# Performance work log

Measured on AMD Instinct MI355X. Metric: run time of the kernel, lower is better.

Reference implementation:

```python
import math
import jax, jax.numpy as jnp
import numpy as np

BLOCK_K = 128  # key/value block size; S_k % BLOCK_K == 0 so no padding/mask needed


def setup_inputs() -> dict:
    key = jax.random.key(0)
    kq, kk, kv = jax.random.split(key, 3)
    B, S, H, Hkv, D = 1, 4096, 16, 8, 128
    return {
        "query": jax.random.normal(kq, (B, S, H, D), dtype=jnp.float32),
        "key": jax.random.normal(kk, (B, S, Hkv, D), dtype=jnp.float32),
        "value": jax.random.normal(kv, (B, S, Hkv, D), dtype=jnp.float32),
    }


def _ring_attention(query, key, value, block_k=BLOCK_K):
    # query: [B, Sq, H, D]; key/value: [B, Sk, Hkv, D]
    scale = 1.0 / math.sqrt(query.shape[-1])
    reps = query.shape[2] // key.shape[2]
    if reps > 1:  # GQA: repeat kv heads to match query heads
        key = jnp.repeat(key, reps, axis=2)
        value = jnp.repeat(value, reps, axis=2)
    q = jnp.transpose(query, (0, 2, 1, 3))   # [B, H, Sq, D]
    k = jnp.transpose(key, (0, 2, 1, 3))     # [B, H, Sk, D]
    v = jnp.transpose(value, (0, 2, 1, 3))
    B, H, Sq, D = q.shape
    Sk = k.shape[2]
    nk = Sk // block_k
    # split keys/values into blocks, block axis leading for scan
    kb = k.reshape(B, H, nk, block_k, D).transpose(2, 0, 1, 3, 4)
    vb = v.reshape(B, H, nk, block_k, D).transpose(2, 0, 1, 3, 4)
    m0 = jnp.full((B, H, Sq), -jnp.inf, dtype=jnp.float32)
    l0 = jnp.zeros((B, H, Sq), dtype=jnp.float32)
    o0 = jnp.zeros((B, H, Sq, D), dtype=jnp.float32)

    def step(carry, kv_blk):
        m, l, o = carry
        k_blk, v_blk = kv_blk
        scores = jnp.einsum('bhqd,bhkd->bhqk', q, k_blk) * scale
        m_new = jnp.maximum(m, jnp.max(scores, axis=-1))
        alpha = jnp.exp(m - m_new)                     # rescale factor (0 on first step)
        p = jnp.exp(scores - m_new[..., None])
        l = l * alpha + jnp.sum(p, axis=-1)
        o = o * alpha[..., None] + jnp.einsum('bhqk,bhkd->bhqd', p, v_blk)
        return (m_new, l, o), None

    (m, l, o), _ = jax.lax.scan(step, (m0, l0, o0), (kb, vb))
    out = o / l[..., None]
    return jnp.transpose(out, (0, 2, 1, 3))  # [B, Sq, H, D]


def reference(query, key, value):
    return _ring_attention(query, key, value)
```

## Files before the change

### kernel.cpp

```cpp
#include <hip/hip_runtime.h>
#include <math.h>


namespace {
constexpr int NH  = 16;
constexpr int NKV = 8;
constexpr int DH  = 128;
constexpr int SK  = 4096;
constexpr int TQ  = 128;
constexpr int NTM = 128;
constexpr int NT  = 256;

constexpr int BKM   = 32;
constexpr int NKTM  = SK / BKM;
constexpr int TILEM = BKM * DH;
constexpr size_t WS_NEED = (size_t)2 * NKV * NKTM * TILEM * sizeof(_Float16);

constexpr int NIT   = NKTM / 2;
constexpr int CHUNK = 2 * TILEM;

constexpr int BK  = 64;
constexpr int NKT = SK / BK;

typedef _Float16 half8 __attribute__((ext_vector_type(8)));
typedef _Float16 half4 __attribute__((ext_vector_type(4)));
typedef _Float16 half2v __attribute__((ext_vector_type(2)));
typedef __fp16   fp16x2 __attribute__((ext_vector_type(2)));
typedef float  floatx4 __attribute__((ext_vector_type(4)));
typedef unsigned short ushort8 __attribute__((ext_vector_type(8)));

#define MFMA16(a, b, c) __builtin_amdgcn_mfma_f32_16x16x32_f16((a), (b), (c), 0, 0, 0)

#define BARRIER_LGKM() asm volatile("s_waitcnt lgkmcnt(0)\n\ts_barrier" ::: "memory")

__global__ __launch_bounds__(256)
void prepack_kv(const float* __restrict__ Kg, const float* __restrict__ Vg,
                _Float16* __restrict__ Kx, _Float16* __restrict__ Vx) {
  __shared__ __align__(16) _Float16 Kb[BKM * 128];
  __shared__ __align__(16) _Float16 Vb[BKM * 132];
  const int id = blockIdx.x;
  const int hk = id & 7;
  const int kt = id >> 3;
  const int t  = threadIdx.x;

#pragma unroll
  for (int it = 0; it < 4; ++it) {
    const int r  = it * 8 + (t >> 5);
    const int c4 = t & 31;
    const size_t src = (((size_t)(kt * BKM + r) * NKV + hk) * DH) + c4 * 4;
    const float4 kf = *reinterpret_cast<const float4*>(Kg + src);
    const float4 vf = *reinterpret_cast<const float4*>(Vg + src);
    half4 kh;
    kh[0] = (_Float16)kf.x; kh[1] = (_Float16)kf.y;
    kh[2] = (_Float16)kf.z; kh[3] = (_Float16)kf.w;
    *reinterpret_cast<half4*>(&Kb[r * 128 + c4 * 4]) = kh;
    half2v v0, v1;
    v0[0] = (_Float16)vf.x; v0[1] = (_Float16)vf.y;
    v1[0] = (_Float16)vf.z; v1[1] = (_Float16)vf.w;
    *reinterpret_cast<half2v*>(&Vb[r * 132 + c4 * 4])     = v0;
    *reinterpret_cast<half2v*>(&Vb[r * 132 + c4 * 4 + 2]) = v1;
  }
  __syncthreads();

  {
    _Float16* out = Kx + (size_t)(hk * NKTM + kt) * TILEM;
#pragma unroll
    for (int it = 0; it < 2; ++it) {
      const int L  = it * 2048 + t * 8;
      const int r  = L >> 7;
      const int gp = (L >> 3) & 15;
      const int c8 = gp ^ (r & 7);
      *reinterpret_cast<half8*>(out + L) =
          *reinterpret_cast<const half8*>(&Kb[r * 128 + c8 * 8]);
    }
  }
  {
    _Float16* out = Vx + (size_t)(hk * NKTM + kt) * TILEM;
    const int dp = t >> 2;
    const int g  = t & 3;
    const int ql = g ^ (dp & 3);
    const int d  = dp * 2;
    ushort8 lo, hi;
#pragma unroll
    for (int j = 0; j < 8; ++j) {
      const int key = ((j >> 2) * 16) + ql * 4 + (j & 3);
      const unsigned v = *reinterpret_cast<const unsigned*>(&Vb[key * 132 + d]);
      lo[j] = (unsigned short)(v & 0xffffu);
      hi[j] = (unsigned short)(v >> 16);
    }
    *reinterpret_cast<ushort8*>(out + d * 32 + g * 8)       = lo;
    *reinterpret_cast<ushort8*>(out + (d + 1) * 32 + g * 8) = hi;
  }
}

__global__ __launch_bounds__(NTM, 1)
void flash_fwd_pk(const float* __restrict__ Qg,
                  const _Float16* __restrict__ Kx,
                  const _Float16* __restrict__ Vx,
                  float* __restrict__ Og) {
  __shared__ __align__(16) _Float16 KsB[2][CHUNK];
  __shared__ __align__(16) _Float16 VtB[2][CHUNK];

  const int tid  = threadIdx.x;
  const int wave = tid >> 6;
  const int lane = tid & 63;
  const int m16  = lane & 15;
  const int quad = lane >> 4;
  const int hsw  = m16 & 7;
  const int sw2  = (m16 >> 1) & 3;

  const int id = blockIdx.x;
  const int hk = id & 7;
  const int h  = (hk << 1) | ((id >> 3) & 1);
  const int qt = id >> 4;
  const int qr0 = qt * TQ + wave * 64;

  const float4* Q4 = reinterpret_cast<const float4*>(Qg);
  const float scale2 = (float)(0.08838834764831845 * 1.4426950408889634);

  half8 qa[4][4];
#pragma unroll
  for (int mt = 0; mt < 4; ++mt) {
#pragma unroll
    for (int kc = 0; kc < 4; ++kc) {
      const int r = qr0 + mt * 16 + m16;
      const int b = (r * NH + h) * (DH / 4) + kc * 8 + quad * 2;
      float4 x = Q4[b], y = Q4[b + 1];
      half8 f;
      f[0] = (_Float16)(x.x * scale2); f[1] = (_Float16)(x.y * scale2);
      f[2] = (_Float16)(x.z * scale2); f[3] = (_Float16)(x.w * scale2);
      f[4] = (_Float16)(y.x * scale2); f[5] = (_Float16)(y.y * scale2);
      f[6] = (_Float16)(y.z * scale2); f[7] = (_Float16)(y.w * scale2);
      qa[mt][kc] = f;
    }
  }

  floatx4 o[4][8];
#pragma unroll
  for (int mt = 0; mt < 4; ++mt)
#pragma unroll
    for (int nt = 0; nt < 8; ++nt) o[mt][nt] = (floatx4){0.f, 0.f, 0.f, 0.f};
  float lsum[4] = {0.f, 0.f, 0.f, 0.f};

  const _Float16* gK = Kx + (size_t)hk * NKTM * TILEM;
  const _Float16* gV = Vx + (size_t)hk * NKTM * TILEM;
  const int soff = tid * 8;

  half8 kr[8], vr[8];
#pragma unroll
  for (int i = 0; i < 8; ++i) {
    kr[i] = *reinterpret_cast<const half8*>(gK + i * 1024 + soff);
    vr[i] = *reinterpret_cast<const half8*>(gV + i * 1024 + soff);
  }

  for (int kt = 0; kt < NIT; ++kt) {
    const int b = kt & 1;
#pragma unroll
    for (int i = 0; i < 8; ++i) {
      *reinterpret_cast<half8*>(&KsB[b][i * 1024 + soff]) = kr[i];
      *reinterpret_cast<half8*>(&VtB[b][i * 1024 + soff]) = vr[i];
    }
    {
      const int ktn = (kt + 1 < NIT) ? kt + 1 : kt;
      const _Float16* gKt = gK + (size_t)ktn * CHUNK;
      const _Float16* gVt = gV + (size_t)ktn * CHUNK;
#pragma unroll
      for (int i = 0; i < 8; ++i) {
        kr[i] = *reinterpret_cast<const half8*>(gKt + i * 1024 + soff);
        vr[i] = *reinterpret_cast<const half8*>(gVt + i * 1024 + soff);
      }
    }
    BARRIER_LGKM();

#pragma unroll
    for (int c = 0; c < 2; ++c) {
      const _Float16* Ks = &KsB[b][c * TILEM];
      const _Float16* Vt = &VtB[b][c * TILEM];

      floatx4 s[4][2];
#pragma unroll
      for (int mt = 0; mt < 4; ++mt)
#pragma unroll
        for (int nt = 0; nt < 2; ++nt) s[mt][nt] = (floatx4){0.f, 0.f, 0.f, 0.f};
#pragma unroll
      for (int nt = 0; nt < 2; ++nt) {
#pragma unroll
        for (int kc = 0; kc < 4; ++kc) {
          const int g = (kc * 4 + quad) ^ hsw;
          half8 kb = *reinterpret_cast<const half8*>(
              &Ks[(nt * 16 + m16) * 128 + g * 8]);
          s[0][nt] = MFMA16(kb, qa[0][kc], s[0][nt]);
          s[1][nt] = MFMA16(kb, qa[1][kc], s[1][nt]);
          s[2][nt] = MFMA16(kb, qa[2][kc], s[2][nt]);
          s[3][nt] = MFMA16(kb, qa[3][kc], s[3][nt]);
        }
      }

      union H8 { half8 h; fp16x2 w[4]; };
      half8 pa[4];
#pragma unroll
      for (int mt = 0; mt < 4; ++mt) {
        float p[8];
#pragma unroll
        for (int nt = 0; nt < 2; ++nt)
#pragma unroll
          for (int r = 0; r < 4; ++r)
            p[nt * 4 + r] = __builtin_amdgcn_exp2f(s[mt][nt][r]);
        lsum[mt] += ((p[0] + p[1]) + (p[2] + p[3])) +
                    ((p[4] + p[5]) + (p[6] + p[7]));
        H8 u;
        u.w[0] = __builtin_amdgcn_cvt_pkrtz(p[0], p[1]);
        u.w[1] = __builtin_amdgcn_cvt_pkrtz(p[2], p[3]);
        u.w[2] = __builtin_amdgcn_cvt_pkrtz(p[4], p[5]);
        u.w[3] = __builtin_amdgcn_cvt_pkrtz(p[6], p[7]);
        pa[mt] = u.h;
      }

      const int gq = quad ^ sw2;
#pragma unroll
      for (int nt = 0; nt < 8; ++nt) {
        half8 vb = *reinterpret_cast<const half8*>(
            &Vt[(nt * 16 + m16) * 32 + gq * 8]);
        o[0][nt] = MFMA16(pa[0], vb, o[0][nt]);
        o[1][nt] = MFMA16(pa[1], vb, o[1][nt]);
        o[2][nt] = MFMA16(pa[2], vb, o[2][nt]);
        o[3][nt] = MFMA16(pa[3], vb, o[3][nt]);
      }
    }
  }

#pragma unroll
  for (int mt = 0; mt < 4; ++mt) {
    float ls = lsum[mt];
    ls += __shfl_xor(ls, 16);
    ls += __shfl_xor(ls, 32);
#pragma unroll
    for (int r = 0; r < 4; ++r) {
      const int rq = quad * 4 + r;
      const float inv = 1.f / __shfl(ls, rq);
      const int row = qr0 + mt * 16 + rq;
      const int ob = (row * NH + h) * DH + m16;
#pragma unroll
      for (int nt = 0; nt < 8; ++nt)
        Og[ob + nt * 16] = o[mt][nt][r] * inv;
    }
  }
}

constexpr int KP = 136, VP = 72, PP = 72;

__global__ __launch_bounds__(NT, 2)
void flash_fwd_fb(const float* __restrict__ Qg, const float* __restrict__ Kg,
                  const float* __restrict__ Vg, float* __restrict__ Og) {
  __shared__ _Float16 Ks[BK * KP];
  __shared__ _Float16 Vt[DH * VP];
  __shared__ _Float16 Ps[4 * 32 * PP];

  const int tid  = threadIdx.x;
  const int wave = tid >> 6;
  const int lane = tid & 63;
  const int m16  = lane & 15;
  const int quad = lane >> 4;

  const int id = blockIdx.x;
  const int hk = id & 7;
  const int h  = (hk << 1) | ((id >> 3) & 1);
  const int qt = id >> 4;
  const int qr0 = qt * TQ + wave * 32;

  const float4* Q4 = reinterpret_cast<const float4*>(Qg);
  const float4* K4 = reinterpret_cast<const float4*>(Kg);
  const float scale2 = (float)(0.08838834764831845 * 1.4426950408889634);

  half8 qa[2][4];
#pragma unroll
  for (int mt = 0; mt < 2; ++mt) {
#pragma unroll
    for (int kc = 0; kc < 4; ++kc) {
      const int r = qr0 + mt * 16 + m16;
      const int b = (r * NH + h) * (DH / 4) + kc * 8 + quad * 2;
      float4 x = Q4[b], y = Q4[b + 1];
      half8 f;
      f[0] = (_Float16)(x.x * scale2); f[1] = (_Float16)(x.y * scale2);
      f[2] = (_Float16)(x.z * scale2); f[3] = (_Float16)(x.w * scale2);
      f[4] = (_Float16)(y.x * scale2); f[5] = (_Float16)(y.y * scale2);
      f[6] = (_Float16)(y.z * scale2); f[7] = (_Float16)(y.w * scale2);
      qa[mt][kc] = f;
    }
  }

  floatx4 o[2][8];
#pragma unroll
  for (int mt = 0; mt < 2; ++mt)
#pragma unroll
    for (int nt = 0; nt < 8; ++nt) o[mt][nt] = (floatx4){0.f, 0.f, 0.f, 0.f};
  float lrow[2][4];
#pragma unroll
  for (int mt = 0; mt < 2; ++mt)
#pragma unroll
    for (int r = 0; r < 4; ++r) lrow[mt][r] = 0.f;

  const int kkey = tid >> 2, kdq = tid & 3;
  const int vdim = tid & 127, vkg = tid >> 7;

  float4 kpre[8];
  float  vpre[32];
  {
    const int kb = (kkey * NKV + hk) * (DH / 4);
#pragma unroll
    for (int j = 0; j < 8; ++j) kpre[j] = K4[kb + j * 4 + kdq];
    const int vb = (vkg * 32) * NKV * DH + hk * DH + vdim;
#pragma unroll
    for (int e = 0; e < 32; ++e) vpre[e] = Vg[vb + e * (NKV * DH)];
  }

  for (int kt = 0; kt < NKT; ++kt) {
    __syncthreads();
#pragma unroll
    for (int j = 0; j < 8; ++j) {
      fp16x2 a = __builtin_amdgcn_cvt_pkrtz(kpre[j].x, kpre[j].y);
      fp16x2 b = __builtin_amdgcn_cvt_pkrtz(kpre[j].z, kpre[j].w);
      half4 hv;
      hv[0] = (_Float16)a[0]; hv[1] = (_Float16)a[1];
      hv[2] = (_Float16)b[0]; hv[3] = (_Float16)b[1];
      *reinterpret_cast<half4*>(&Ks[kkey * KP + (j * 4 + kdq) * 4]) = hv;
    }
#pragma unroll
    for (int jj = 0; jj < 4; ++jj) {
      half8 hv;
#pragma unroll
      for (int e = 0; e < 4; ++e) {
        fp16x2 p = __builtin_amdgcn_cvt_pkrtz(vpre[jj * 8 + 2 * e],
                                              vpre[jj * 8 + 2 * e + 1]);
        hv[2 * e] = (_Float16)p[0]; hv[2 * e + 1] = (_Float16)p[1];
      }
      *reinterpret_cast<half8*>(&Vt[vdim * VP + vkg * 32 + jj * 8]) = hv;
    }
    __syncthreads();

    floatx4 s[2][4];
#pragma unroll
    for (int mt = 0; mt < 2; ++mt)
#pragma unroll
      for (int nt = 0; nt < 4; ++nt) s[mt][nt] = (floatx4){0.f, 0.f, 0.f, 0.f};
#pragma unroll
    for (int nt = 0; nt < 4; ++nt) {
#pragma unroll
      for (int kc = 0; kc < 4; ++kc) {
        half8 kb = *reinterpret_cast<const half8*>(
            &Ks[(nt * 16 + m16) * KP + kc * 32 + quad * 8]);
        s[0][nt] = MFMA16(qa[0][kc], kb, s[0][nt]);
        s[1][nt] = MFMA16(qa[1][kc], kb, s[1][nt]);
      }
    }

    {
      const int ktn = (kt + 1 < NKT) ? kt + 1 : kt;
      const int kb = ((ktn * BK + kkey) * NKV + hk) * (DH / 4);
#pragma unroll
      for (int j = 0; j < 8; ++j) kpre[j] = K4[kb + j * 4 + kdq];
      const int vb = (ktn * BK + vkg * 32) * NKV * DH + hk * DH + vdim;
#pragma unroll
      for (int e = 0; e < 32; ++e) vpre[e] = Vg[vb + e * (NKV * DH)];
    }

#pragma unroll
    for (int mt = 0; mt < 2; ++mt) {
#pragma unroll
      for (int nt = 0; nt < 4; ++nt) {
#pragma unroll
        for (int r = 0; r < 4; ++r) {
          const float p = exp2f(s[mt][nt][r]);
          s[mt][nt][r] = p;
          lrow[mt][r] += p;
        }
      }
#pragma unroll
      for (int r = 0; r < 4; ++r) {
        const int prow = (wave * 32 + mt * 16 + quad * 4 + r) * PP;
#pragma unroll
        for (int nt = 0; nt < 4; ++nt)
          Ps[prow + nt * 16 + m16] = (_Float16)s[mt][nt][r];
      }
    }

    half8 pa[2][2];
#pragma unroll
    for (int mt = 0; mt < 2; ++mt)
#pragma unroll
      for (int kc = 0; kc < 2; ++kc)
        pa[mt][kc] = *reinterpret_cast<const half8*>(
            &Ps[(wave * 32 + mt * 16 + m16) * PP + kc * 32 + quad * 8]);
#pragma unroll
    for (int nt = 0; nt < 8; ++nt) {
#pragma unroll
      for (int kc = 0; kc < 2; ++kc) {
        half8 vb = *reinterpret_cast<const half8*>(
            &Vt[(nt * 16 + m16) * VP + kc * 32 + quad * 8]);
        o[0][nt] = MFMA16(pa[0][kc], vb, o[0][nt]);
        o[1][nt] = MFMA16(pa[1][kc], vb, o[1][nt]);
      }
    }
  }

#pragma unroll
  for (int mt = 0; mt < 2; ++mt) {
#pragma unroll
    for (int r = 0; r < 4; ++r) {
      float ls = lrow[mt][r];
      ls += __shfl_xor(ls, 1);
      ls += __shfl_xor(ls, 2);
      ls += __shfl_xor(ls, 4);
      ls += __shfl_xor(ls, 8);
      const float inv = 1.f / ls;
      const int row = qr0 + mt * 16 + quad * 4 + r;
      const int ob = (row * NH + h) * DH + m16;
#pragma unroll
      for (int nt = 0; nt < 8; ++nt)
        Og[ob + nt * 16] = o[mt][nt][r] * inv;
    }
  }
}
}

extern "C" void kernel_launch(void* const* d_in, const int* in_sizes, int n_in,
                              void* d_out, int out_size, void* d_ws, size_t ws_size,
                              hipStream_t stream) {
  const float* Q = (const float*)d_in[0];
  const float* K = (const float*)d_in[1];
  const float* V = (const float*)d_in[2];
  float* O = (float*)d_out;
  if (ws_size >= WS_NEED) {
    _Float16* Kx = (_Float16*)d_ws;
    _Float16* Vx = Kx + (size_t)NKV * NKTM * TILEM;
    prepack_kv<<<1024, 256, 0, stream>>>(K, V, Kx, Vx);
    flash_fwd_pk<<<512, NTM, 0, stream>>>(Q, Kx, Vx, O);
  } else {
    flash_fwd_fb<<<512, NT, 0, stream>>>(Q, K, V, O);
  }
}
```

Baseline: 262.2 us.

## Split key range across two wave groups per block with shared-memory reduction

Each block now runs 256 threads in two wave groups. Each group processes half of the key tiles for the same 128 query rows, and the partial outputs and row sums are merged through shared memory at the end. This doubles the waves available per block to hide latency from MFMA, exp and LDS work, at the cost of an extra reduction step, more register pressure under the 2-blocks-per-SM launch bound, and per-group LDS buffers.

```diff
diff --git a/kernel.cpp b/kernel.cpp
--- a/kernel.cpp
+++ b/kernel.cpp
@@ -8,7 +8,6 @@
 constexpr int DH  = 128;
 constexpr int SK  = 4096;
 constexpr int TQ  = 128;
-constexpr int NTM = 128;
 constexpr int NT  = 256;
 
 constexpr int BKM   = 32;
@@ -16,8 +15,7 @@
 constexpr int TILEM = BKM * DH;
 constexpr size_t WS_NEED = (size_t)2 * NKV * NKTM * TILEM * sizeof(_Float16);
 
-constexpr int NIT   = NKTM / 2;
-constexpr int CHUNK = 2 * TILEM;
+constexpr int NITG = NKTM / 2;
 
 constexpr int BK  = 64;
 constexpr int NKT = SK / BK;
@@ -93,16 +91,19 @@
   }
 }
 
-__global__ __launch_bounds__(NTM, 1)
+__global__ __launch_bounds__(NT, 2)
 void flash_fwd_pk(const float* __restrict__ Qg,
                   const _Float16* __restrict__ Kx,
                   const _Float16* __restrict__ Vx,
                   float* __restrict__ Og) {
-  __shared__ __align__(16) _Float16 KsB[2][CHUNK];
-  __shared__ __align__(16) _Float16 VtB[2][CHUNK];
+  __shared__ __align__(16) _Float16 KsB[2][2][TILEM];
+  __shared__ __align__(16) _Float16 VtB[2][2][TILEM];
+  __shared__ float Lx[2][64][4];
 
   const int tid  = threadIdx.x;
   const int wave = tid >> 6;
+  const int grp  = wave >> 1;
+  const int wq   = wave & 1;
   const int lane = tid & 63;
   const int m16  = lane & 15;
   const int quad = lane >> 4;
@@ -113,7 +114,7 @@
   const int hk = id & 7;
   const int h  = (hk << 1) | ((id >> 3) & 1);
   const int qt = id >> 4;
-  const int qr0 = qt * TQ + wave * 64;
+  const int qr0 = qt * TQ + wq * 64;
 
   const float4* Q4 = reinterpret_cast<const float4*>(Qg);
   const float scale2 = (float)(0.08838834764831845 * 1.4426950408889634);
@@ -142,107 +143,129 @@
     for (int nt = 0; nt < 8; ++nt) o[mt][nt] = (floatx4){0.f, 0.f, 0.f, 0.f};
   float lsum[4] = {0.f, 0.f, 0.f, 0.f};
 
-  const _Float16* gK = Kx + (size_t)hk * NKTM * TILEM;
-  const _Float16* gV = Vx + (size_t)hk * NKTM * TILEM;
-  const int soff = tid * 8;
-
-  half8 kr[8], vr[8];
-#pragma unroll
-  for (int i = 0; i < 8; ++i) {
+  const _Float16* gK = Kx + ((size_t)hk * NKTM + (size_t)grp * NITG) * TILEM;
+  const _Float16* gV = Vx + ((size_t)hk * NKTM + (size_t)grp * NITG) * TILEM;
+  const int soff = (wq * 64 + lane) * 8;
+
+  half8 kr[4], vr[4];
+#pragma unroll
+  for (int i = 0; i < 4; ++i) {
     kr[i] = *reinterpret_cast<const half8*>(gK + i * 1024 + soff);
     vr[i] = *reinterpret_cast<const half8*>(gV + i * 1024 + soff);
   }
 
-  for (int kt = 0; kt < NIT; ++kt) {
+  for (int kt = 0; kt < NITG; ++kt) {
     const int b = kt & 1;
 #pragma unroll
-    for (int i = 0; i < 8; ++i) {
-      *reinterpret_cast<half8*>(&KsB[b][i * 1024 + soff]) = kr[i];
-      *reinterpret_cast<half8*>(&VtB[b][i * 1024 + soff]) = vr[i];
+    for (int i = 0; i < 4; ++i) {
+      *reinterpret_cast<half8*>(&KsB[grp][b][i * 1024 + soff]) = kr[i];
+      *reinterpret_cast<half8*>(&VtB[grp][b][i * 1024 + soff]) = vr[i];
     }
     {
-      const int ktn = (kt + 1 < NIT) ? kt + 1 : kt;
-      const _Float16* gKt = gK + (size_t)ktn * CHUNK;
-      const _Float16* gVt = gV + (size_t)ktn * CHUNK;
-#pragma unroll
-      for (int i = 0; i < 8; ++i) {
+      const int ktn = (kt + 1 < NITG) ? kt + 1 : kt;
+      const _Float16* gKt = gK + (size_t)ktn * TILEM;
+      const _Float16* gVt = gV + (size_t)ktn * TILEM;
+#pragma unroll
+      for (int i = 0; i < 4; ++i) {
         kr[i] = *reinterpret_cast<const half8*>(gKt + i * 1024 + soff);
         vr[i] = *reinterpret_cast<const half8*>(gVt + i * 1024 + soff);
       }
     }
     BARRIER_LGKM();
 
-#pragma unroll
-    for (int c = 0; c < 2; ++c) {
-      const _Float16* Ks = &KsB[b][c * TILEM];
-      const _Float16* Vt = &VtB[b][c * TILEM];
-
-      floatx4 s[4][2];
-#pragma unroll
-      for (int mt = 0; mt < 4; ++mt)
-#pragma unroll
-        for (int nt = 0; nt < 2; ++nt) s[mt][nt] = (floatx4){0.f, 0.f, 0.f, 0.f};
-#pragma unroll
-      for (int nt = 0; nt < 2; ++nt) {
-#pragma unroll
-        for (int kc = 0; kc < 4; ++kc) {
-          const int g = (kc * 4 + quad) ^ hsw;
-          half8 kb = *reinterpret_cast<const half8*>(
-              &Ks[(nt * 16 + m16) * 128 + g * 8]);
-          s[0][nt] = MFMA16(kb, qa[0][kc], s[0][nt]);
-          s[1][nt] = MFMA16(kb, qa[1][kc], s[1][nt]);
-          s[2][nt] = MFMA16(kb, qa[2][kc], s[2][nt]);
-          s[3][nt] = MFMA16(kb, qa[3][kc], s[3][nt]);
-        }
-      }
-
-      union H8 { half8 h; fp16x2 w[4]; };
-      half8 pa[4];
-#pragma unroll
-      for (int mt = 0; mt < 4; ++mt) {
-        float p[8];
-#pragma unroll
-        for (int nt = 0; nt < 2; ++nt)
-#pragma unroll
-          for (int r = 0; r < 4; ++r)
-            p[nt * 4 + r] = __builtin_amdgcn_exp2f(s[mt][nt][r]);
-        lsum[mt] += ((p[0] + p[1]) + (p[2] + p[3])) +
-                    ((p[4] + p[5]) + (p[6] + p[7]));
-        H8 u;
-        u.w[0] = __builtin_amdgcn_cvt_pkrtz(p[0], p[1]);
-        u.w[1] = __builtin_amdgcn_cvt_pkrtz(p[2], p[3]);
-        u.w[2] = __builtin_amdgcn_cvt_pkrtz(p[4], p[5]);
-        u.w[3] = __builtin_amdgcn_cvt_pkrtz(p[6], p[7]);
-        pa[mt] = u.h;
-      }
-
-      const int gq = quad ^ sw2;
+    const _Float16* Ks = KsB[grp][b];
+    const _Float16* Vt = VtB[grp][b];
+
+    floatx4 s[4][2];
+#pragma unroll
+    for (int mt = 0; mt < 4; ++mt)
+#pragma unroll
+      for (int nt = 0; nt < 2; ++nt) s[mt][nt] = (floatx4){0.f, 0.f, 0.f, 0.f};
+#pragma unroll
+    for (int nt = 0; nt < 2; ++nt) {
+#pragma unroll
+      for (int kc = 0; kc < 4; ++kc) {
+        const int g = (kc * 4 + quad) ^ hsw;
+        half8 kb = *reinterpret_cast<const half8*>(
+            &Ks[(nt * 16 + m16) * 128 + g * 8]);
+        s[0][nt] = MFMA16(kb, qa[0][kc], s[0][nt]);
+        s[1][nt] = MFMA16(kb, qa[1][kc], s[1][nt]);
+        s[2][nt] = MFMA16(kb, qa[2][kc], s[2][nt]);
+        s[3][nt] = MFMA16(kb, qa[3][kc], s[3][nt]);
+      }
+    }
+
+    union H8 { half8 h; fp16x2 w[4]; };
+    half8 pa[4];
+#pragma unroll
+    for (int mt = 0; mt < 4; ++mt) {
+      float p[8];
+#pragma unroll
+      for (int nt = 0; nt < 2; ++nt)
+#pragma unroll
+        for (int r = 0; r < 4; ++r)
+          p[nt * 4 + r] = __builtin_amdgcn_exp2f(s[mt][nt][r]);
+      lsum[mt] += ((p[0] + p[1]) + (p[2] + p[3])) +
+                  ((p[4] + p[5]) + (p[6] + p[7]));
+      H8 u;
+      u.w[0] = __builtin_amdgcn_cvt_pkrtz(p[0], p[1]);
+      u.w[1] = __builtin_amdgcn_cvt_pkrtz(p[2], p[3]);
+      u.w[2] = __builtin_amdgcn_cvt_pkrtz(p[4], p[5]);
+      u.w[3] = __builtin_amdgcn_cvt_pkrtz(p[6], p[7]);
+      pa[mt] = u.h;
+    }
+
+    const int gq = quad ^ sw2;
+#pragma unroll
+    for (int nt = 0; nt < 8; ++nt) {
+      half8 vb = *reinterpret_cast<const half8*>(
+          &Vt[(nt * 16 + m16) * 32 + gq * 8]);
+      o[0][nt] = MFMA16(pa[0], vb, o[0][nt]);
+      o[1][nt] = MFMA16(pa[1], vb, o[1][nt]);
+      o[2][nt] = MFMA16(pa[2], vb, o[2][nt]);
+      o[3][nt] = MFMA16(pa[3], vb, o[3][nt]);
+    }
+  }
+
+  __syncthreads();
+  floatx4* osc = reinterpret_cast<floatx4*>(
+      wq == 0 ? (void*)&KsB[0][0][0] : (void*)&VtB[0][0][0]);
+  if (grp == 1) {
+#pragma unroll
+    for (int mt = 0; mt < 4; ++mt) {
+#pragma unroll
+      for (int nt = 0; nt < 8; ++nt)
+        osc[(mt * 8 + nt) * 64 + lane] = o[mt][nt];
+      Lx[wq][lane][mt] = lsum[mt];
+    }
+  }
+  __syncthreads();
+  if (grp == 0) {
+#pragma unroll
+    for (int mt = 0; mt < 4; ++mt) {
+      lsum[mt] += Lx[wq][lane][mt];
 #pragma unroll
       for (int nt = 0; nt < 8; ++nt) {
-        half8 vb = *reinterpret_cast<const half8*>(
-            &Vt[(nt * 16 + m16) * 32 + gq * 8]);
-        o[0][nt] = MFMA16(pa[0], vb, o[0][nt]);
-        o[1][nt] = MFMA16(pa[1], vb, o[1][nt]);
-        o[2][nt] = MFMA16(pa[2], vb, o[2][nt]);
-        o[3][nt] = MFMA16(pa[3], vb, o[3][nt]);
-      }
-    }
-  }
-
-#pragma unroll
-  for (int mt = 0; mt < 4; ++mt) {
-    float ls = lsum[mt];
-    ls += __shfl_xor(ls, 16);
-    ls += __shfl_xor(ls, 32);
-#pragma unroll
-    for (int r = 0; r < 4; ++r) {
-      const int rq = quad * 4 + r;
-      const float inv = 1.f / __shfl(ls, rq);
-      const int row = qr0 + mt * 16 + rq;
-      const int ob = (row * NH + h) * DH + m16;
-#pragma unroll
-      for (int nt = 0; nt < 8; ++nt)
-        Og[ob + nt * 16] = o[mt][nt][r] * inv;
+        const floatx4 t = osc[(mt * 8 + nt) * 64 + lane];
+        o[mt][nt][0] += t[0]; o[mt][nt][1] += t[1];
+        o[mt][nt][2] += t[2]; o[mt][nt][3] += t[3];
+      }
+    }
+#pragma unroll
+    for (int mt = 0; mt < 4; ++mt) {
+      float ls = lsum[mt];
+      ls += __shfl_xor(ls, 16);
+      ls += __shfl_xor(ls, 32);
+#pragma unroll
+      for (int r = 0; r < 4; ++r) {
+        const int rq = quad * 4 + r;
+        const float inv = 1.f / __shfl(ls, rq);
+        const int row = qr0 + mt * 16 + rq;
+        const int ob = (row * NH + h) * DH + m16;
+#pragma unroll
+        for (int nt = 0; nt < 8; ++nt)
+          Og[ob + nt * 16] = o[mt][nt][r] * inv;
+      }
     }
   }
 }
@@ -434,7 +457,7 @@
     _Float16* Kx = (_Float16*)d_ws;
     _Float16* Vx = Kx + (size_t)NKV * NKTM * TILEM;
     prepack_kv<<<1024, 256, 0, stream>>>(K, V, Kx, Vx);
-    flash_fwd_pk<<<512, NTM, 0, stream>>>(Q, Kx, Vx, O);
+    flash_fwd_pk<<<512, NT, 0, stream>>>(Q, Kx, Vx, O);
   } else {
     flash_fwd_fb<<<512, NT, 0, stream>>>(Q, K, V, O);
   }
```

Result: slower. 398.1 us (+51.8%).
